# Kernel tuning notes

Measured on AMD Instinct MI355X. Metric: run time of the kernel, lower is better.

The kernel has to match this reference:

```python
import jax, jax.numpy as jnp
import numpy as np

N_NODES = 50000
N_EDGES = 800000
D_IN = 128
D_HID = 128
D_OUT = 64


def sage_conv(x, edge_index, W_l, b_l, W_r):
    # PyG SAGEConv (mean aggr): out = lin_l(mean_{j in N(i)} x_j) + lin_r(x_i)
    src, dst = edge_index[0], edge_index[1]
    msgs = x[src]  # [E, d] gather of source-node features
    summed = jax.ops.segment_sum(msgs, dst, num_segments=x.shape[0])
    deg = jax.ops.segment_sum(jnp.ones((edge_index.shape[1],), x.dtype), dst,
                              num_segments=x.shape[0])
    agg = summed / jnp.maximum(deg, 1.0)[:, None]  # nodes w/o in-edges -> 0
    return agg @ W_l + b_l + x @ W_r


def setup_inputs() -> dict:
    key = jax.random.key(0)
    ks = jax.random.split(key, 12)
    x = jax.random.normal(ks[0], (N_NODES, D_IN), dtype=jnp.float32)
    edge_index = jax.random.randint(ks[1], (2, N_EDGES), 0, N_NODES, dtype=jnp.int32)

    def glorot(k, shape):
        fan_in, fan_out = shape
        lim = (6.0 / (fan_in + fan_out)) ** 0.5
        return jax.random.uniform(k, shape, jnp.float32, -lim, lim)

    dims = [(D_IN, D_HID), (D_HID, D_HID), (D_HID, D_OUT)]
    params = {}
    for i, (din, dout) in enumerate(dims):
        params[f"Wl{i}"] = glorot(ks[2 + 3 * i], (din, dout))
        params[f"bl{i}"] = jnp.zeros((dout,), jnp.float32)
        params[f"Wr{i}"] = glorot(ks[3 + 3 * i], (din, dout))
    return {"x": x, "edge_index": edge_index, **params}


def reference(x, edge_index, Wl0, bl0, Wr0, Wl1, bl1, Wr1, Wl2, bl2, Wr2):
    # eval mode: dropout is identity
    h = jax.nn.relu(sage_conv(x, edge_index, Wl0, bl0, Wr0))
    h = jax.nn.relu(sage_conv(h, edge_index, Wl1, bl1, Wr1))
    out = sage_conv(h, edge_index, Wl2, bl2, Wr2)
    return out
```

## Files before the change

kernel.cpp:

```cpp
#include <hip/hip_runtime.h>

#define NN 50000
#define NE 800000
#define DK 128
#define NN_PAD 50048

#define SW 7
#define SUBCAP 20
#define CAP2 64

#define NPB 128
#define NBKT 391
#define BKTCAP 4096

#define GEMM_GRID 391

#define AGG_BLOCKS 1568

typedef __attribute__((ext_vector_type(8))) short bf16x8;
typedef __attribute__((ext_vector_type(4))) float f32x4;
typedef __attribute__((ext_vector_type(2))) int   i32x2;
typedef __attribute__((ext_vector_type(4))) int   i32x4;
typedef __attribute__((ext_vector_type(4))) unsigned u32x4;
typedef __attribute__((ext_vector_type(8))) unsigned short u16x8;

__device__ inline unsigned short f2bf(float f) {
    unsigned u = __builtin_bit_cast(unsigned, f);
    u = (u + 0x7FFFu + ((u >> 16) & 1u)) >> 16;
    return (unsigned short)u;
}
__device__ inline float bfhi2f(unsigned u) {
    return __builtin_bit_cast(float, u & 0xFFFF0000u);
}
__device__ inline float bflo2f(unsigned u) {
    return __builtin_bit_cast(float, u << 16);
}
__device__ inline int clampn(int v) {
    return v >= NN ? NN - 1 : v;
}
__device__ inline void acc16(float* acc, u32x4 v) {
    acc[0] += bflo2f(v.x); acc[1] += bfhi2f(v.x);
    acc[2] += bflo2f(v.y); acc[3] += bfhi2f(v.y);
    acc[4] += bflo2f(v.z); acc[5] += bfhi2f(v.z);
    acc[6] += bflo2f(v.w); acc[7] += bfhi2f(v.w);
}


__global__ __launch_bounds__(256) void partition_edges(const int* __restrict__ src,
                                                       const int* __restrict__ dst,
                                                       int* __restrict__ gcount,
                                                       unsigned* __restrict__ bucketbuf) {
    __shared__ int hist[NBKT];
    __shared__ int cur[NBKT];
    __shared__ int base[NBKT];
    int tid = threadIdx.x;
    for (int i = tid; i < NBKT; i += 256) { hist[i] = 0; cur[i] = 0; }
    __syncthreads();

    unsigned rec[8];
    int bkt[8];
    int e0 = (blockIdx.x * 256 + tid) * 8;
    bool valid = e0 < NE;
    if (valid) {
        i32x4 sa = __builtin_nontemporal_load((const i32x4*)(src + e0));
        i32x4 sb = __builtin_nontemporal_load((const i32x4*)(src + e0 + 4));
        i32x4 da = __builtin_nontemporal_load((const i32x4*)(dst + e0));
        i32x4 db = __builtin_nontemporal_load((const i32x4*)(dst + e0 + 4));
        int ss[8] = {sa.x, sa.y, sa.z, sa.w, sb.x, sb.y, sb.z, sb.w};
        int dd[8] = {da.x, da.y, da.z, da.w, db.x, db.y, db.z, db.w};
        #pragma unroll
        for (int k = 0; k < 8; ++k) {
            bkt[k] = dd[k] >> 7;
            rec[k] = (unsigned)ss[k] | ((unsigned)(dd[k] & 127) << 16);
            atomicAdd(&hist[bkt[k]], 1);
        }
    }
    __syncthreads();
    for (int i = tid; i < NBKT; i += 256)
        base[i] = atomicAdd(&gcount[i], hist[i]);
    __syncthreads();
    if (valid) {
        #pragma unroll
        for (int k = 0; k < 8; ++k) {
            int pos = base[bkt[k]] + atomicAdd(&cur[bkt[k]], 1);
            if (pos < BKTCAP)
                bucketbuf[(size_t)bkt[k] * BKTCAP + pos] = rec[k];
        }
    }
}

__global__ __launch_bounds__(256) void build_lists(const int* __restrict__ gcount,
                                                   const unsigned* __restrict__ bucketbuf,
                                                   unsigned short* __restrict__ eidx2,
                                                   int* __restrict__ deg) {
    __shared__ unsigned short list[NPB * CAP2];
    __shared__ int cnt[NPB * 8];
    __shared__ int cur[NPB * 8];
    __shared__ int off_[NPB * 8];
    int b = blockIdx.x, tid = threadIdx.x;
    int n0 = b << 7;
    int cntE = gcount[b];
    if (cntE > BKTCAP) cntE = BKTCAP;

    for (int i = tid; i < NPB * 8; i += 256) { cnt[i] = 0; cur[i] = 0; }
    u32x4* l4 = (u32x4*)list;
    for (int i = tid; i < NPB * CAP2 / 8; i += 256)
        l4[i] = (u32x4){0u, 0u, 0u, 0u};
    __syncthreads();

    const unsigned* bb = bucketbuf + (size_t)b * BKTCAP;
    for (int i = tid; i < cntE; i += 256) {
        unsigned r = bb[i];
        int nl = r >> 16;
        int w  = (r & 0xFFFFu) >> 13;
        atomicAdd(&cnt[nl * 8 + w], 1);
    }
    __syncthreads();

    if (tid < NPB) {
        int run = 0, dt = 0;
        #pragma unroll
        for (int w = 0; w < SW; ++w) {
            int c = cnt[tid * 8 + w];
            dt += c;
            off_[tid * 8 + w] = run;
            run += (c < SUBCAP) ? c : SUBCAP;
        }
        if (n0 + tid < NN) deg[n0 + tid] = dt;
    }
    __syncthreads();

    for (int i = tid; i < cntE; i += 256) {
        unsigned r = bb[i];
        int s  = (int)(r & 0xFFFFu);
        int nl = r >> 16;
        int w  = s >> 13;
        int slot = atomicAdd(&cur[nl * 8 + w], 1);
        int pos  = off_[nl * 8 + w] + slot;
        if (slot < SUBCAP && pos < CAP2)
            list[nl * CAP2 + pos] = (unsigned short)s;
    }
    __syncthreads();

    int nvalid = NN - n0;
    if (nvalid > NPB) nvalid = NPB;
    u32x4* out4 = (u32x4*)(eidx2 + (size_t)n0 * CAP2);
    for (int i = tid; i < nvalid * (CAP2 / 8); i += 256)
        __builtin_nontemporal_store(l4[i], out4 + i);
}

__global__ __launch_bounds__(256) void prep(const float* __restrict__ x,
                                            unsigned short* __restrict__ xb,
                                            const float* __restrict__ Wl0,
                                            const float* __restrict__ Wr0,
                                            unsigned short* __restrict__ Wp0,
                                            const float* __restrict__ Wl1,
                                            const float* __restrict__ Wr1,
                                            unsigned short* __restrict__ Wp1,
                                            const float* __restrict__ Wl2,
                                            unsigned short* __restrict__ Wp2l,
                                            const float* __restrict__ Wr2,
                                            unsigned short* __restrict__ Wp2r,
                                            int* __restrict__ gcount) {
    int b = blockIdx.x;
    if (b < NN_PAD * DK / 8 / 256) {
        long long i = ((long long)b * 256 + threadIdx.x) * 8;
        if (i < (long long)NN * DK) {
            f32x4 a = __builtin_nontemporal_load((const f32x4*)(x + i));
            f32x4 c = __builtin_nontemporal_load((const f32x4*)(x + i + 4));
            union { unsigned short us[8]; u32x4 u4; } o;
            o.us[0] = f2bf(a.x); o.us[1] = f2bf(a.y); o.us[2] = f2bf(a.z); o.us[3] = f2bf(a.w);
            o.us[4] = f2bf(c.x); o.us[5] = f2bf(c.y); o.us[6] = f2bf(c.z); o.us[7] = f2bf(c.w);
            *(u32x4*)(xb + i) = o.u4;
        } else {
            *(u32x4*)(xb + i) = (u32x4){0u, 0u, 0u, 0u};
        }
        return;
    }
    b -= NN_PAD * DK / 8 / 256;
    if (b < 32) {
        const float* Wl = (b < 16) ? Wl0 : Wl1;
        const float* Wr = (b < 16) ? Wr0 : Wr1;
        unsigned short* Wp = (b < 16) ? Wp0 : Wp1;
        int tid = (b & 15) * 256 + threadIdx.x;
        int l  = tid & 63;
        int ks = (tid >> 6) & 7;
        int nt = tid >> 9;
        int n  = nt * 16 + (l & 15);
        int kb = ks * 32 + (l >> 4) * 8;
        union { unsigned short us[8]; u32x4 u4; } o;
        #pragma unroll
        for (int j = 0; j < 8; ++j) {
            int k = kb + j;
            float w = (k < 128) ? Wl[k * 128 + n] : Wr[(k - 128) * 128 + n];
            o.us[j] = f2bf(w);
        }
        *(u32x4*)(Wp + (size_t)tid * 8) = o.u4;
        return;
    }
    b -= 32;
    if (b < 8) {
        const float* W = (b < 4) ? Wl2 : Wr2;
        unsigned short* Wp = (b < 4) ? Wp2l : Wp2r;
        int tid = (b & 3) * 256 + threadIdx.x;
        int l  = tid & 63;
        int ks = (tid >> 6) & 3;
        int nt = tid >> 8;
        int n  = nt * 16 + (l & 15);
        int kb = ks * 32 + (l >> 4) * 8;
        union { unsigned short us[8]; u32x4 u4; } o;
        #pragma unroll
        for (int j = 0; j < 8; ++j) o.us[j] = f2bf(W[(kb + j) * 64 + n]);
        *(u32x4*)(Wp + (size_t)tid * 8) = o.u4;
        return;
    }
    for (int i = threadIdx.x; i < NBKT; i += 256) gcount[i] = 0;
}

template <int S>
__global__ __launch_bounds__(256) void aggregate(const unsigned short* __restrict__ h,
                                                 const unsigned short* __restrict__ eidx2,
                                                 const int* __restrict__ deg,
                                                 unsigned short* __restrict__ agg) {
    constexpr int NPB_ = 256 / S;
    int g    = threadIdx.x / S;
    int lane = threadIdx.x % S;
    const u32x4* h4 = (const u32x4*)h;
    for (int base = 0; base < NN; base += AGG_BLOCKS * NPB_) {
        int node = base + blockIdx.x * NPB_ + g;
        if (node >= NN) continue;
        int d   = deg[node];
        int cap = (d < CAP2) ? d : CAP2;
        const unsigned short* el = eidx2 + (size_t)node * CAP2;
        float acc[8] = {0.f, 0.f, 0.f, 0.f, 0.f, 0.f, 0.f, 0.f};
        int j = 0;
        for (; j + 7 < cap; j += 8) {
            u16x8 i8 = *(const u16x8*)(el + j);
            u32x4 v[8];
            #pragma unroll
            for (int q = 0; q < 8; ++q)
                v[q] = h4[(size_t)clampn((int)i8[q]) * S + lane];
            #pragma unroll
            for (int q = 0; q < 8; ++q) acc16(acc, v[q]);
        }
        for (; j + 3 < cap; j += 4) {
            u32x4 v[4];
            #pragma unroll
            for (int q = 0; q < 4; ++q)
                v[q] = h4[(size_t)clampn((int)el[j + q]) * S + lane];
            #pragma unroll
            for (int q = 0; q < 4; ++q) acc16(acc, v[q]);
        }
        for (; j < cap; ++j)
            acc16(acc, h4[(size_t)clampn((int)el[j]) * S + lane]);
        float r = 1.0f / (float)(d > 0 ? d : 1);
        union { unsigned short us[8]; u32x4 u4; } o;
        #pragma unroll
        for (int k = 0; k < 8; ++k) o.us[k] = f2bf(acc[k] * r);
        __builtin_nontemporal_store(o.u4, (u32x4*)agg + (size_t)node * S + lane);
    }
}


template <bool P2OUT>
__global__ __launch_bounds__(256) void gemm_mfma(const unsigned short* __restrict__ agg,
                                                 const unsigned short* __restrict__ h,
                                                 const unsigned short* __restrict__ Wpack,
                                                 const float* __restrict__ bias,
                                                 unsigned short* __restrict__ out,
                                                 const unsigned short* __restrict__ Wp2,
                                                 unsigned short* __restrict__ P2) {
    __shared__ unsigned short Wlds[128 * 256];
    int tid = threadIdx.x;
    {
        const u32x4* wg = (const u32x4*)Wpack;
        u32x4* wl = (u32x4*)Wlds;
        #pragma unroll
        for (int i = tid; i < 128 * 32; i += 256) wl[i] = wg[i];
    }
    __syncthreads();

    int wave = tid >> 6, lane = tid & 63;
    int m = lane & 15, quad = lane >> 4;
    int r0 = wave * 16;
    int row0 = blockIdx.x * 128 + r0;

    const unsigned short* arow = agg + (size_t)(row0 + m) * 128 + quad * 8;
    const unsigned short* hrow = h   + (size_t)(row0 + m) * 128 + quad * 8;

    f32x4 acc0[8] = {};
    f32x4 acc1[8] = {};
    #pragma unroll
    for (int ks = 0; ks < 8; ++ks) {
        const unsigned short* s = (ks < 4) ? (arow + ks * 32) : (hrow + (ks - 4) * 32);
        bf16x8 a0 = *(const bf16x8*)s;
        bf16x8 a1 = *(const bf16x8*)(s + 64 * 128);
        #pragma unroll
        for (int nt = 0; nt < 8; ++nt) {
            bf16x8 b = *(const bf16x8*)&Wlds[((nt * 8 + ks) * 64 + lane) * 8];
            acc0[nt] = __builtin_amdgcn_mfma_f32_16x16x32_bf16(a0, b, acc0[nt], 0, 0, 0);
            acc1[nt] = __builtin_amdgcn_mfma_f32_16x16x32_bf16(a1, b, acc1[nt], 0, 0, 0);
        }
    }

    #pragma unroll
    for (int t = 0; t < 2; ++t) {
        #pragma unroll
        for (int nt = 0; nt < 8; ++nt) {
            int n = nt * 16 + m;
            float bv = bias[n];
            #pragma unroll
            for (int r = 0; r < 4; ++r) {
                int row = row0 + t * 64 + quad * 4 + r;
                if (row < NN) {
                    float v = fmaxf((t == 0 ? acc0[nt][r] : acc1[nt][r]) + bv, 0.f);
                    out[(size_t)row * 128 + n] = f2bf(v);
                }
            }
        }
    }

    if constexpr (P2OUT) {
        constexpr int RS = 136;
        __syncthreads();
        #pragma unroll
        for (int t = 0; t < 2; ++t) {
            #pragma unroll
            for (int nt = 0; nt < 8; ++nt) {
                int n = nt * 16 + m;
                float bv = bias[n];
                #pragma unroll
                for (int r = 0; r < 4; ++r) {
                    int rl = t * 64 + r0 + quad * 4 + r;
                    float v = fmaxf((t == 0 ? acc0[nt][r] : acc1[nt][r]) + bv, 0.f);
                    Wlds[rl * RS + n] = f2bf(v);
                }
            }
        }
        f32x4 p0[4] = {};
        f32x4 p1[4] = {};
        #pragma unroll
        for (int ks = 0; ks < 4; ++ks) {
            bf16x8 a0 = *(const bf16x8*)&Wlds[(r0 + m) * RS + ks * 32 + quad * 8];
            bf16x8 a1 = *(const bf16x8*)&Wlds[(64 + r0 + m) * RS + ks * 32 + quad * 8];
            #pragma unroll
            for (int nt = 0; nt < 4; ++nt) {
                bf16x8 bfr = *(const bf16x8*)&Wp2[((size_t)(nt * 4 + ks) * 64 + lane) * 8];
                p0[nt] = __builtin_amdgcn_mfma_f32_16x16x32_bf16(a0, bfr, p0[nt], 0, 0, 0);
                p1[nt] = __builtin_amdgcn_mfma_f32_16x16x32_bf16(a1, bfr, p1[nt], 0, 0, 0);
            }
        }
        #pragma unroll
        for (int t = 0; t < 2; ++t) {
            #pragma unroll
            for (int nt = 0; nt < 4; ++nt) {
                int n = nt * 16 + m;
                #pragma unroll
                for (int r = 0; r < 4; ++r) {
                    int rl = t * 64 + r0 + quad * 4 + r;
                    P2[(size_t)(blockIdx.x * 128 + rl) * 64 + n] =
                        f2bf(t == 0 ? p0[nt][r] : p1[nt][r]);
                }
            }
        }
    }
}

__global__ __launch_bounds__(256) void gemm_final(const unsigned short* __restrict__ h,
                                                  const unsigned short* __restrict__ Wpack,
                                                  const float* __restrict__ bias,
                                                  const unsigned short* __restrict__ aggP,
                                                  float* __restrict__ outp) {
    __shared__ unsigned short Wlds[64 * 128];
    int tid = threadIdx.x;
    {
        const u32x4* wg = (const u32x4*)Wpack;
        u32x4* wl = (u32x4*)Wlds;
        #pragma unroll
        for (int i = tid; i < 1024; i += 256) wl[i] = wg[i];
    }
    __syncthreads();

    int wave = tid >> 6, lane = tid & 63;
    int m = lane & 15, quad = lane >> 4;
    int row0 = blockIdx.x * 128 + wave * 16;

    const unsigned short* hrow = h + (size_t)(row0 + m) * 128 + quad * 8;

    f32x4 acc0[4] = {};
    f32x4 acc1[4] = {};
    #pragma unroll
    for (int ks = 0; ks < 4; ++ks) {
        bf16x8 a0 = *(const bf16x8*)(hrow + ks * 32);
        bf16x8 a1 = *(const bf16x8*)(hrow + ks * 32 + 64 * 128);
        #pragma unroll
        for (int nt = 0; nt < 4; ++nt) {
            bf16x8 b = *(const bf16x8*)&Wlds[((nt * 4 + ks) * 64 + lane) * 8];
            acc0[nt] = __builtin_amdgcn_mfma_f32_16x16x32_bf16(a0, b, acc0[nt], 0, 0, 0);
            acc1[nt] = __builtin_amdgcn_mfma_f32_16x16x32_bf16(a1, b, acc1[nt], 0, 0, 0);
        }
    }

    #pragma unroll
    for (int t = 0; t < 2; ++t) {
        #pragma unroll
        for (int nt = 0; nt < 4; ++nt) {
            int n = nt * 16 + m;
            float bv = bias[n];
            #pragma unroll
            for (int r = 0; r < 4; ++r) {
                int row = row0 + t * 64 + quad * 4 + r;
                if (row < NN) {
                    float av = bflo2f((unsigned)aggP[(size_t)row * 64 + n]);
                    outp[(size_t)row * 64 + n] =
                        (t == 0 ? acc0[nt][r] : acc1[nt][r]) + bv + av;
                }
            }
        }
    }
}


static inline size_t align256(size_t x) { return (x + 255) & ~(size_t)255; }

extern "C" void kernel_launch(void* const* d_in, const int* in_sizes, int n_in,
                              void* d_out, int out_size, void* d_ws, size_t ws_size,
                              hipStream_t stream) {
    const float* x    = (const float*)d_in[0];
    const int*   ei   = (const int*)d_in[1];
    const int*   esrc = ei;
    const int*   edst = ei + NE;
    const float* Wl0 = (const float*)d_in[2];
    const float* bl0 = (const float*)d_in[3];
    const float* Wr0 = (const float*)d_in[4];
    const float* Wl1 = (const float*)d_in[5];
    const float* bl1 = (const float*)d_in[6];
    const float* Wr1 = (const float*)d_in[7];
    const float* Wl2 = (const float*)d_in[8];
    const float* bl2 = (const float*)d_in[9];
    const float* Wr2 = (const float*)d_in[10];

    char* ws = (char*)d_ws;
    size_t off = 0;
    int* gcount = (int*)(ws + off);             off = align256(off + (size_t)NBKT * 4);
    unsigned* bucketbuf = (unsigned*)(ws + off);
    off = align256(off + (size_t)NBKT * BKTCAP * 4);
    unsigned short* eidx2 = (unsigned short*)(ws + off);
    off = align256(off + (size_t)NN * CAP2 * 2);
    int* deg = (int*)(ws + off);                off = align256(off + (size_t)NN * 4);
    unsigned short* xb   = (unsigned short*)(ws + off); off = align256(off + (size_t)NN_PAD * DK * 2);
    unsigned short* bAgg = (unsigned short*)(ws + off); off = align256(off + (size_t)NN_PAD * DK * 2);
    unsigned short* bH   = (unsigned short*)(ws + off); off = align256(off + (size_t)NN_PAD * DK * 2);
    unsigned short* P2   = (unsigned short*)(ws + off); off = align256(off + (size_t)NN_PAD * 64 * 2);
    unsigned short* aggP = (unsigned short*)(ws + off); off = align256(off + (size_t)NN_PAD * 64 * 2);
    unsigned short* Wp0  = (unsigned short*)(ws + off); off = align256(off + (size_t)256 * 128 * 2);
    unsigned short* Wp1  = (unsigned short*)(ws + off); off = align256(off + (size_t)256 * 128 * 2);
    unsigned short* Wp2l = (unsigned short*)(ws + off); off = align256(off + (size_t)128 * 64 * 2);
    unsigned short* Wp2r = (unsigned short*)(ws + off); off = align256(off + (size_t)128 * 64 * 2);

    prep<<<NN_PAD * DK / 8 / 256 + 32 + 8 + 1, 256, 0, stream>>>(
        x, xb, Wl0, Wr0, Wp0, Wl1, Wr1, Wp1, Wl2, Wp2l, Wr2, Wp2r, gcount);
    partition_edges<<<(NE / 8 + 255) / 256, 256, 0, stream>>>(esrc, edst, gcount, bucketbuf);
    build_lists<<<NBKT, 256, 0, stream>>>(gcount, bucketbuf, eidx2, deg);

    aggregate<16><<<AGG_BLOCKS, 256, 0, stream>>>(xb, eidx2, deg, bAgg);
    gemm_mfma<false><<<GEMM_GRID, 256, 0, stream>>>(bAgg, xb, Wp0, bl0, bH,
                                                    nullptr, nullptr);

    aggregate<16><<<AGG_BLOCKS, 256, 0, stream>>>(bH, eidx2, deg, bAgg);
    gemm_mfma<true><<<GEMM_GRID, 256, 0, stream>>>(bAgg, bH, Wp1, bl1, xb,
                                                   Wp2l, P2);

    aggregate<8><<<AGG_BLOCKS, 256, 0, stream>>>(P2, eidx2, deg, aggP);
    gemm_final<<<GEMM_GRID, 256, 0, stream>>>(xb, Wp2r, bl2, aggP, (float*)d_out);
}
```

Measured before the change: 240.1 us.

## Halve GEMM tile to 64 rows and read weights from global instead of LDS

```diff
diff --git a/kernel.cpp b/kernel.cpp
--- a/kernel.cpp
+++ b/kernel.cpp
@@ -13,7 +13,7 @@
 #define NBKT 391
 #define BKTCAP 4096
 
-#define GEMM_GRID 391
+#define GEMM_GRID 782
 
 #define AGG_BLOCKS 1568
 
@@ -270,97 +270,64 @@
                                                  unsigned short* __restrict__ out,
                                                  const unsigned short* __restrict__ Wp2,
                                                  unsigned short* __restrict__ P2) {
-    __shared__ unsigned short Wlds[128 * 256];
+    constexpr int RS = 136;
+    __shared__ unsigned short Alds[P2OUT ? 64 * RS : 8];
     int tid = threadIdx.x;
-    {
-        const u32x4* wg = (const u32x4*)Wpack;
-        u32x4* wl = (u32x4*)Wlds;
-        #pragma unroll
-        for (int i = tid; i < 128 * 32; i += 256) wl[i] = wg[i];
-    }
-    __syncthreads();
-
     int wave = tid >> 6, lane = tid & 63;
     int m = lane & 15, quad = lane >> 4;
     int r0 = wave * 16;
-    int row0 = blockIdx.x * 128 + r0;
-
-    const unsigned short* arow = agg + (size_t)(row0 + m) * 128 + quad * 8;
-    const unsigned short* hrow = h   + (size_t)(row0 + m) * 128 + quad * 8;
+    int node0 = blockIdx.x * 64;
+
+    const unsigned short* arow = agg + (size_t)(node0 + r0 + m) * 128 + quad * 8;
+    const unsigned short* hrow = h   + (size_t)(node0 + r0 + m) * 128 + quad * 8;
+    const bf16x8* wp = (const bf16x8*)Wpack + lane;
 
     f32x4 acc0[8] = {};
-    f32x4 acc1[8] = {};
     #pragma unroll
     for (int ks = 0; ks < 8; ++ks) {
         const unsigned short* s = (ks < 4) ? (arow + ks * 32) : (hrow + (ks - 4) * 32);
         bf16x8 a0 = *(const bf16x8*)s;
-        bf16x8 a1 = *(const bf16x8*)(s + 64 * 128);
         #pragma unroll
         for (int nt = 0; nt < 8; ++nt) {
-            bf16x8 b = *(const bf16x8*)&Wlds[((nt * 8 + ks) * 64 + lane) * 8];
+            bf16x8 b = wp[(nt * 8 + ks) * 64];
             acc0[nt] = __builtin_amdgcn_mfma_f32_16x16x32_bf16(a0, b, acc0[nt], 0, 0, 0);
-            acc1[nt] = __builtin_amdgcn_mfma_f32_16x16x32_bf16(a1, b, acc1[nt], 0, 0, 0);
         }
     }
 
     #pragma unroll
-    for (int t = 0; t < 2; ++t) {
-        #pragma unroll
-        for (int nt = 0; nt < 8; ++nt) {
+    for (int nt = 0; nt < 8; ++nt) {
+        int n = nt * 16 + m;
+        float bv = bias[n];
+        #pragma unroll
+        for (int r = 0; r < 4; ++r) {
+            int rl = r0 + quad * 4 + r;
+            int row = node0 + rl;
+            float v = fmaxf(acc0[nt][r] + bv, 0.f);
+            unsigned short us = f2bf(v);
+            if (row < NN) out[(size_t)row * 128 + n] = us;
+            if constexpr (P2OUT) Alds[rl * RS + n] = us;
+        }
+    }
+
+    if constexpr (P2OUT) {
+        const bf16x8* wp2 = (const bf16x8*)Wp2 + lane;
+        f32x4 p0[4] = {};
+        #pragma unroll
+        for (int ks = 0; ks < 4; ++ks) {
+            bf16x8 a0 = *(const bf16x8*)&Alds[(r0 + m) * RS + ks * 32 + quad * 8];
+            #pragma unroll
+            for (int nt = 0; nt < 4; ++nt)
+                p0[nt] = __builtin_amdgcn_mfma_f32_16x16x32_bf16(a0, wp2[(nt * 4 + ks) * 64],
+                                                                 p0[nt], 0, 0, 0);
+        }
+        #pragma unroll
+        for (int nt = 0; nt < 4; ++nt) {
             int n = nt * 16 + m;
-            float bv = bias[n];
             #pragma unroll
             for (int r = 0; r < 4; ++r) {
-                int row = row0 + t * 64 + quad * 4 + r;
-                if (row < NN) {
-                    float v = fmaxf((t == 0 ? acc0[nt][r] : acc1[nt][r]) + bv, 0.f);
-                    out[(size_t)row * 128 + n] = f2bf(v);
-                }
-            }
-        }
-    }
-
-    if constexpr (P2OUT) {
-        constexpr int RS = 136;
-        __syncthreads();
-        #pragma unroll
-        for (int t = 0; t < 2; ++t) {
-            #pragma unroll
-            for (int nt = 0; nt < 8; ++nt) {
-                int n = nt * 16 + m;
-                float bv = bias[n];
-                #pragma unroll
-                for (int r = 0; r < 4; ++r) {
-                    int rl = t * 64 + r0 + quad * 4 + r;
-                    float v = fmaxf((t == 0 ? acc0[nt][r] : acc1[nt][r]) + bv, 0.f);
-                    Wlds[rl * RS + n] = f2bf(v);
-                }
-            }
-        }
-        f32x4 p0[4] = {};
-        f32x4 p1[4] = {};
-        #pragma unroll
-        for (int ks = 0; ks < 4; ++ks) {
-            bf16x8 a0 = *(const bf16x8*)&Wlds[(r0 + m) * RS + ks * 32 + quad * 8];
-            bf16x8 a1 = *(const bf16x8*)&Wlds[(64 + r0 + m) * RS + ks * 32 + quad * 8];
-            #pragma unroll
-            for (int nt = 0; nt < 4; ++nt) {
-                bf16x8 bfr = *(const bf16x8*)&Wp2[((size_t)(nt * 4 + ks) * 64 + lane) * 8];
-                p0[nt] = __builtin_amdgcn_mfma_f32_16x16x32_bf16(a0, bfr, p0[nt], 0, 0, 0);
-                p1[nt] = __builtin_amdgcn_mfma_f32_16x16x32_bf16(a1, bfr, p1[nt], 0, 0, 0);
-            }
-        }
-        #pragma unroll
-        for (int t = 0; t < 2; ++t) {
-            #pragma unroll
-            for (int nt = 0; nt < 4; ++nt) {
-                int n = nt * 16 + m;
-                #pragma unroll
-                for (int r = 0; r < 4; ++r) {
-                    int rl = t * 64 + r0 + quad * 4 + r;
-                    P2[(size_t)(blockIdx.x * 128 + rl) * 64 + n] =
-                        f2bf(t == 0 ? p0[nt][r] : p1[nt][r]);
-                }
+                int rl = r0 + quad * 4 + r;
+                int row = node0 + rl;
+                if (row < NN) P2[(size_t)row * 64 + n] = f2bf(p0[nt][r]);
             }
         }
     }
@@ -371,50 +338,35 @@
                                                   const float* __restrict__ bias,
                                                   const unsigned short* __restrict__ aggP,
                                                   float* __restrict__ outp) {
-    __shared__ unsigned short Wlds[64 * 128];
     int tid = threadIdx.x;
-    {
-        const u32x4* wg = (const u32x4*)Wpack;
-        u32x4* wl = (u32x4*)Wlds;
-        #pragma unroll
-        for (int i = tid; i < 1024; i += 256) wl[i] = wg[i];
-    }
-    __syncthreads();
-
     int wave = tid >> 6, lane = tid & 63;
     int m = lane & 15, quad = lane >> 4;
-    int row0 = blockIdx.x * 128 + wave * 16;
-
-    const unsigned short* hrow = h + (size_t)(row0 + m) * 128 + quad * 8;
+    int r0 = wave * 16;
+    int node0 = blockIdx.x * 64;
+
+    const unsigned short* hrow = h + (size_t)(node0 + r0 + m) * 128 + quad * 8;
+    const bf16x8* wp = (const bf16x8*)Wpack + lane;
 
     f32x4 acc0[4] = {};
-    f32x4 acc1[4] = {};
     #pragma unroll
     for (int ks = 0; ks < 4; ++ks) {
         bf16x8 a0 = *(const bf16x8*)(hrow + ks * 32);
-        bf16x8 a1 = *(const bf16x8*)(hrow + ks * 32 + 64 * 128);
-        #pragma unroll
-        for (int nt = 0; nt < 4; ++nt) {
-            bf16x8 b = *(const bf16x8*)&Wlds[((nt * 4 + ks) * 64 + lane) * 8];
-            acc0[nt] = __builtin_amdgcn_mfma_f32_16x16x32_bf16(a0, b, acc0[nt], 0, 0, 0);
-            acc1[nt] = __builtin_amdgcn_mfma_f32_16x16x32_bf16(a1, b, acc1[nt], 0, 0, 0);
-        }
+        #pragma unroll
+        for (int nt = 0; nt < 4; ++nt)
+            acc0[nt] = __builtin_amdgcn_mfma_f32_16x16x32_bf16(a0, wp[(nt * 4 + ks) * 64],
+                                                               acc0[nt], 0, 0, 0);
     }
 
     #pragma unroll
-    for (int t = 0; t < 2; ++t) {
-        #pragma unroll
-        for (int nt = 0; nt < 4; ++nt) {
-            int n = nt * 16 + m;
-            float bv = bias[n];
-            #pragma unroll
-            for (int r = 0; r < 4; ++r) {
-                int row = row0 + t * 64 + quad * 4 + r;
-                if (row < NN) {
-                    float av = bflo2f((unsigned)aggP[(size_t)row * 64 + n]);
-                    outp[(size_t)row * 64 + n] =
-                        (t == 0 ? acc0[nt][r] : acc1[nt][r]) + bv + av;
-                }
+    for (int nt = 0; nt < 4; ++nt) {
+        int n = nt * 16 + m;
+        float bv = bias[n];
+        #pragma unroll
+        for (int r = 0; r < 4; ++r) {
+            int row = node0 + r0 + quad * 4 + r;
+            if (row < NN) {
+                float av = bflo2f((unsigned)aggP[(size_t)row * 64 + n]);
+                outp[(size_t)row * 64 + n] = acc0[nt][r] + bv + av;
             }
         }
     }
```

After: 246.0 us. 2.5% more time.
